# Kernel tuning notes

Hardware: AMD Instinct MI355X
Metric: run time of the kernel (lower is better)

The kernel has to match this reference:

```python
import jax, jax.numpy as jnp
import numpy as np

H = 16       # num heads
D = 80       # head dim
HID = H * D  # 1280
S = 4096     # total tokens


def setup_inputs() -> dict:
    key = jax.random.key(0)
    ks = jax.random.split(key, 6)
    x = jax.random.normal(ks[0], (S, HID), dtype=jnp.float32)
    # 4 images of 1024 patch tokens each
    cu_seqlens = jnp.array([0, 1024, 2048, 3072, 4096], dtype=jnp.int32)
    rotary_pos_emb = jax.random.normal(ks[1], (S, D // 2), dtype=jnp.float32)
    sc = 1.0 / np.sqrt(HID)
    qkv_w = jax.random.normal(ks[2], (3 * HID, HID), dtype=jnp.float32) * sc
    qkv_b = jax.random.normal(ks[3], (3 * HID,), dtype=jnp.float32) * 0.02
    proj_w = jax.random.normal(ks[4], (HID, HID), dtype=jnp.float32) * sc
    proj_b = jax.random.normal(ks[5], (HID,), dtype=jnp.float32) * 0.02
    return {"x": x, "cu_seqlens": cu_seqlens, "rotary_pos_emb": rotary_pos_emb,
            "qkv_w": qkv_w, "qkv_b": qkv_b, "proj_w": proj_w, "proj_b": proj_b}


def _rotate_half(t):
    t1, t2 = jnp.split(t, 2, axis=-1)
    return jnp.concatenate([-t2, t1], axis=-1)


def _apply_rope(t, freqs):
    # t: [S, H, D], freqs: [S, D//2] -> cos/sin broadcast as [S, 1, D]
    emb = jnp.concatenate([freqs, freqs], axis=-1)[:, None, :]
    return t * jnp.cos(emb) + _rotate_half(t) * jnp.sin(emb)


def reference(x, cu_seqlens, rotary_pos_emb, qkv_w, qkv_b, proj_w, proj_b):
    seq_len = x.shape[0]
    qkv = (x @ qkv_w.T + qkv_b).reshape(seq_len, 3, H, D)
    q, k, v = qkv[:, 0], qkv[:, 1], qkv[:, 2]  # each [S, H, D]
    q = _apply_rope(q, rotary_pos_emb)
    k = _apply_rope(k, rotary_pos_emb)
    # block-diagonal mask from cu_seqlens: same segment -> 0, else dtype min
    seg = jnp.searchsorted(cu_seqlens[1:], jnp.arange(seq_len), side='right')
    neg = jnp.finfo(q.dtype).min
    attn_mask = jnp.where(seg[:, None] == seg[None, :], 0.0, neg).astype(q.dtype)
    scores = jnp.einsum('shd,thd->hst', q, k) / jnp.sqrt(jnp.asarray(D, q.dtype))
    scores = scores + attn_mask[None]
    attn = jax.nn.softmax(scores.astype(jnp.float32), axis=-1).astype(q.dtype)
    out = jnp.einsum('hst,thd->shd', attn, v).reshape(seq_len, H * D)
    return out @ proj_w.T + proj_b
```

## Files before the change

kernel.cpp:

```cpp
#include <hip/hip_runtime.h>

typedef _Float16 f16;
typedef __attribute__((ext_vector_type(8))) _Float16 f16x8;
typedef __attribute__((ext_vector_type(4))) float f32x4;

#define SEQ   4096
#define NH    16
#define HD    80
#define HIDN  1280
#define DP    96

#define KSZ   3328
#define VSZ   4480
#define HSZ   (2*KSZ + 2*VSZ)

#define KQ   1280
#define NQ   3840
#define NIT  10

__device__ __forceinline__ void gload16(const void* g, void* l) {
  __builtin_amdgcn_global_load_lds(
      (const __attribute__((address_space(1))) unsigned int*)g,
      (__attribute__((address_space(3))) unsigned int*)l, 16, 0, 0);
}

__device__ __forceinline__ unsigned pk2(float a, float b) {
  return __builtin_bit_cast(unsigned, __builtin_amdgcn_cvt_pkrtz(a, b));
}
__device__ __forceinline__ f16x8 bc16(uint4 u) { return __builtin_bit_cast(f16x8, u); }

#define BAR() __builtin_amdgcn_s_barrier()
#define VMCNT(n) do { asm volatile("s_waitcnt vmcnt(" #n ")" ::: "memory"); \
                      __builtin_amdgcn_sched_barrier(0); } while (0)
#define STG(Lb, g, buf, h, kt)                                                  \
  do {                                                                          \
    gload16((g) + (size_t)((h) * 128) * KQ + (kt) * 64,                         \
            (Lb) + (buf) * 16384 + ((h) * 128) * 64 + w * 512);                 \
    gload16((g) + (size_t)((h) * 128 + 64) * KQ + (kt) * 64,                    \
            (Lb) + (buf) * 16384 + ((h) * 128 + 64) * 64 + w * 512);            \
  } while (0)
#define MFQ(IOFF, JOFF, BB)                                                     \
  do {                                                                          \
    __builtin_amdgcn_s_setprio(1);                                              \
    _Pragma("unroll")                                                           \
    for (int i_ = 0; i_ < 4; i_++)                                              \
      _Pragma("unroll")                                                         \
      for (int j_ = 0; j_ < 2; j_++)                                            \
        _Pragma("unroll")                                                       \
        for (int s_ = 0; s_ < 2; s_++)                                          \
          acc[i_ + IOFF][j_ + JOFF] = __builtin_amdgcn_mfma_f32_16x16x32_f16(   \
              a[i_][s_], BB[j_][s_], acc[i_ + IOFF][j_ + JOFF], 0, 0, 0);       \
    __builtin_amdgcn_s_setprio(0);                                              \
  } while (0)

__global__ __launch_bounds__(256) void cvt3_kernel(const float* __restrict__ s0,
                                                   const float* __restrict__ s1,
                                                   const float* __restrict__ s2,
                                                   f16* __restrict__ d0,
                                                   f16* __restrict__ d1,
                                                   f16* __restrict__ d2,
                                                   int n0, int n1, int n2) {
  long i = (long)(blockIdx.x * 256 + threadIdx.x) * 8;
  const float* s; f16* d;
  if (i < n0)                { s = s0 + i;            d = d0 + i; }
  else if (i < n0 + n1)      { s = s1 + (i - n0);     d = d1 + (i - n0); }
  else if (i < n0 + n1 + n2) { s = s2 + (i - n0 - n1); d = d2 + (i - n0 - n1); }
  else return;
  f32x4 v0 = *(const f32x4*)(s);
  f32x4 v1 = *(const f32x4*)(s + 4);
  f16x8 o;
#pragma unroll
  for (int j = 0; j < 4; j++) { o[j] = (f16)v0[j]; o[4 + j] = (f16)v1[j]; }
  *(f16x8*)(d) = o;
}

__global__ __launch_bounds__(512, 2) void qkv_gemm8(const f16* __restrict__ A,
                                                    const f16* __restrict__ B,
                                                    const float* __restrict__ bias,
                                                    f16* __restrict__ C) {
  __shared__ __align__(16) f16 LA[2 * 16384];
  __shared__ __align__(16) f16 LB[2 * 16384];
  const int tid = threadIdx.x, w = tid >> 6, l = tid & 63;
  const int bid = (blockIdx.x & 7) * 30 + (blockIdx.x >> 3);
  const int bx = bid % 15, by = bid / 15;
  const int m0 = by * 256, n0 = bx * 256;
  const int wm = (w >> 2) * 128, wn = (w & 3) * 64;
  const int fr = l & 15, fq = l >> 4;
  const int rx = fr & 7;
  const int cA0 = (fq ^ rx) * 8;
  const int cA1 = ((4 + fq) ^ rx) * 8;

  const int srow = w * 8 + (l >> 3);
  const int scol = ((l & 7) ^ (l >> 3)) * 8;
  const f16* gA = A + (size_t)(m0 + srow) * KQ + scol;
  const f16* gB = B + (size_t)(n0 + srow) * KQ + scol;

  f32x4 acc[8][4] = {};
  f16x8 a[4][2], b0[2][2], b1[2][2];

  STG(LA, gA, 0, 0, 0); STG(LA, gA, 0, 1, 0);
  STG(LB, gB, 0, 0, 0); STG(LB, gB, 0, 1, 0);
  STG(LB, gB, 1, 0, 1); STG(LB, gB, 1, 1, 1);
  VMCNT(4);
  BAR();

  for (int it = 0; it < NIT; ++it) {
    const int t = 2 * it;
    const bool lastit = (it == NIT - 1);

#pragma unroll
    for (int i = 0; i < 4; i++) {
      a[i][0] = *(const f16x8*)(LA + (wm + i * 16 + fr) * 64 + cA0);
      a[i][1] = *(const f16x8*)(LA + (wm + i * 16 + fr) * 64 + cA1);
    }
#pragma unroll
    for (int j = 0; j < 2; j++) {
      b0[j][0] = *(const f16x8*)(LB + (wn + j * 16 + fr) * 64 + cA0);
      b0[j][1] = *(const f16x8*)(LB + (wn + j * 16 + fr) * 64 + cA1);
    }
    STG(LA, gA, 1, 0, t + 1);
    BAR(); MFQ(0, 0, b0); BAR();

#pragma unroll
    for (int j = 0; j < 2; j++) {
      b1[j][0] = *(const f16x8*)(LB + (wn + 32 + j * 16 + fr) * 64 + cA0);
      b1[j][1] = *(const f16x8*)(LB + (wn + 32 + j * 16 + fr) * 64 + cA1);
    }
    STG(LA, gA, 1, 1, t + 1);
    BAR(); MFQ(0, 2, b1); BAR();

#pragma unroll
    for (int i = 0; i < 4; i++) {
      a[i][0] = *(const f16x8*)(LA + (wm + 64 + i * 16 + fr) * 64 + cA0);
      a[i][1] = *(const f16x8*)(LA + (wm + 64 + i * 16 + fr) * 64 + cA1);
    }
    if (!lastit) { STG(LB, gB, 0, 0, t + 2); }
    BAR(); MFQ(4, 0, b0); BAR();

    if (!lastit) { STG(LB, gB, 0, 1, t + 2); VMCNT(4); }
    else         { VMCNT(0); }
    BAR(); MFQ(4, 2, b1); BAR();

#pragma unroll
    for (int i = 0; i < 4; i++) {
      a[i][0] = *(const f16x8*)(LA + 16384 + (wm + i * 16 + fr) * 64 + cA0);
      a[i][1] = *(const f16x8*)(LA + 16384 + (wm + i * 16 + fr) * 64 + cA1);
    }
#pragma unroll
    for (int j = 0; j < 2; j++) {
      b0[j][0] = *(const f16x8*)(LB + 16384 + (wn + j * 16 + fr) * 64 + cA0);
      b0[j][1] = *(const f16x8*)(LB + 16384 + (wn + j * 16 + fr) * 64 + cA1);
    }
    if (!lastit) { STG(LA, gA, 0, 0, t + 2); }
    BAR(); MFQ(0, 0, b0); BAR();

#pragma unroll
    for (int j = 0; j < 2; j++) {
      b1[j][0] = *(const f16x8*)(LB + 16384 + (wn + 32 + j * 16 + fr) * 64 + cA0);
      b1[j][1] = *(const f16x8*)(LB + 16384 + (wn + 32 + j * 16 + fr) * 64 + cA1);
    }
    if (!lastit) { STG(LA, gA, 0, 1, t + 2); }
    BAR(); MFQ(0, 2, b1); BAR();

#pragma unroll
    for (int i = 0; i < 4; i++) {
      a[i][0] = *(const f16x8*)(LA + 16384 + (wm + 64 + i * 16 + fr) * 64 + cA0);
      a[i][1] = *(const f16x8*)(LA + 16384 + (wm + 64 + i * 16 + fr) * 64 + cA1);
    }
    if (!lastit) { STG(LB, gB, 1, 0, t + 3); }
    BAR(); MFQ(4, 0, b0); BAR();

    if (!lastit) { STG(LB, gB, 1, 1, t + 3); VMCNT(4); }
    BAR(); MFQ(4, 2, b1); BAR();
  }

#pragma unroll
  for (int i = 0; i < 8; i++) {
    const int row = m0 + wm + i * 16 + fq * 4;
#pragma unroll
    for (int j = 0; j < 4; j++) {
      const int col = n0 + wn + j * 16 + fr;
      const float bv = bias[col];
#pragma unroll
      for (int q = 0; q < 4; q++)
        C[(size_t)(row + q) * NQ + col] = (f16)(acc[i][j][q] + bv);
    }
  }
}

template<int OUT_F32>
__global__ __launch_bounds__(256) void gemm_bt64(const f16* __restrict__ A,
                                                 const f16* __restrict__ B,
                                                 const float* __restrict__ bias,
                                                 void* __restrict__ C,
                                                 int M, int N, int K) {
  __shared__ __align__(16) f16 AsF[8192];
  __shared__ __align__(16) f16 BsF[8192];
  const int tid = threadIdx.x;
  const int w = tid >> 6, l = tid & 63;
  const int m0 = blockIdx.y * 128, n0 = blockIdx.x * 128;
  const int wm = (w >> 1) * 64, wn = (w & 1) * 64;
  const int fr = l & 15, fg = (l >> 4) * 8;

  size_t aoff[4], boff[4];
#pragma unroll
  for (int i = 0; i < 4; i++) {
    const int d = i * 256 + tid;
    const int sub = d >> 9, dd = d & 511;
    const int r = dd >> 2, c = (dd & 3) + sub * 4;
    aoff[i] = (size_t)(m0 + r) * K + c * 8;
    boff[i] = (size_t)(n0 + r) * K + c * 8;
  }

  f32x4 acc[4][4] = {};

  for (int k0 = 0; k0 < K; k0 += 64) {
    if (k0) __syncthreads();
#pragma unroll
    for (int i = 0; i < 4; i++) gload16(A + aoff[i] + k0, AsF + (i * 256 + tid) * 8);
#pragma unroll
    for (int i = 0; i < 4; i++) gload16(B + boff[i] + k0, BsF + (i * 256 + tid) * 8);
    __syncthreads();
    f16x8 af[4][2], bf[4][2];
#pragma unroll
    for (int i = 0; i < 4; i++)
#pragma unroll
      for (int s = 0; s < 2; s++) {
        af[i][s] = *(const f16x8*)(AsF + s * 4096 + (wm + i * 16 + fr) * 32 + fg);
        bf[i][s] = *(const f16x8*)(BsF + s * 4096 + (wn + i * 16 + fr) * 32 + fg);
      }
#pragma unroll
    for (int i = 0; i < 4; i++)
#pragma unroll
      for (int j = 0; j < 4; j++)
#pragma unroll
        for (int s = 0; s < 2; s++)
          acc[i][j] = __builtin_amdgcn_mfma_f32_16x16x32_f16(af[i][s], bf[j][s], acc[i][j], 0, 0, 0);
  }

  const int q4 = (l >> 4) * 4;
#pragma unroll
  for (int i = 0; i < 4; i++) {
    const int row = m0 + wm + i * 16 + q4;
#pragma unroll
    for (int j = 0; j < 4; j++) {
      const int col = n0 + wn + j * 16 + fr;
      const float bv = bias[col];
#pragma unroll
      for (int q = 0; q < 4; q++) {
        float v = acc[i][j][q] + bv;
        if (OUT_F32) ((float*)C)[(size_t)(row + q) * N + col] = v;
        else         ((f16*)C)[(size_t)(row + q) * N + col] = (f16)v;
      }
    }
  }
}

#define RPB 1280
__global__ __launch_bounds__(256) void prep_kernel(const f16* __restrict__ qkvb,
                                                   const float* __restrict__ rpe,
                                                   f16* __restrict__ qh,
                                                   f16* __restrict__ kh,
                                                   f16* __restrict__ vt) {
  __shared__ f16 tile[HD][65];
  const int b = blockIdx.x;
  if (b < RPB) {
    const float SCLT = 0.1118033988749895f * 1.4426950408889634f;
    const int t = b * 256 + threadIdx.x;
    const int d8 = (t % 5) * 8;
    const int h = (t / 5) % NH;
    const int s = t / (5 * NH);
    const f32x4 f0 = *(const f32x4*)(rpe + s * 40 + d8);
    const f32x4 f1 = *(const f32x4*)(rpe + s * 40 + d8 + 4);
    const f16* base = qkvb + (size_t)s * (3 * HIDN) + h * HD;
    const f16x8 q0 = *(const f16x8*)(base + d8);
    const f16x8 q1 = *(const f16x8*)(base + 40 + d8);
    const f16x8 k0 = *(const f16x8*)(base + HIDN + d8);
    const f16x8 k1 = *(const f16x8*)(base + HIDN + 40 + d8);
    f16x8 oq0, oq1, ok0, ok1;
#pragma unroll
    for (int j = 0; j < 8; j++) {
      const float fv = (j < 4) ? f0[j] : f1[j - 4];
      float sn, cs;
      __sincosf(fv, &sn, &cs);
      const float a = (float)q0[j], bq = (float)q1[j];
      oq0[j] = (f16)((a * cs - bq * sn) * SCLT);
      oq1[j] = (f16)((bq * cs + a * sn) * SCLT);
      const float ka = (float)k0[j], kb = (float)k1[j];
      ok0[j] = (f16)(ka * cs - kb * sn);
      ok1[j] = (f16)(kb * cs + ka * sn);
    }
    const size_t ob = ((size_t)h * SEQ + s) * DP;
    *(f16x8*)(qh + ob + d8)      = oq0;
    *(f16x8*)(qh + ob + 40 + d8) = oq1;
    *(f16x8*)(kh + ob + d8)      = ok0;
    *(f16x8*)(kh + ob + 40 + d8) = ok1;
    if (d8 == 32) {
      const f16x8 z = {};
      *(f16x8*)(qh + ob + 80) = z; *(f16x8*)(qh + ob + 88) = z;
      *(f16x8*)(kh + ob + 80) = z; *(f16x8*)(kh + ob + 88) = z;
    }
  } else {
    const int bb = b - RPB;
    const int h = bb >> 6;
    const int s0 = (bb & 63) * 64;
    for (int idx = threadIdx.x; idx < 64 * HD; idx += 256) {
      const int sr = idx / HD, d = idx % HD;
      tile[d][sr] = qkvb[(size_t)(s0 + sr) * (3 * HIDN) + 2 * HIDN + h * HD + d];
    }
    __syncthreads();
    for (int idx = threadIdx.x; idx < HD * 64; idx += 256) {
      const int d = idx >> 6, sc = idx & 63;
      const int blk = sc >> 5, s = sc & 31, g = s >> 3, j = s & 7;
      const int act = blk * 32 + ((j < 4) ? (4 * g + j) : (16 + 4 * g + (j - 4)));
      vt[((size_t)h * HD + d) * SEQ + s0 + sc] = tile[d][act];
    }
  }
}

__global__ __launch_bounds__(512, 2) void attn_kernel(const f16* __restrict__ qh,
                                                      const f16* __restrict__ kh,
                                                      const f16* __restrict__ vt,
                                                      const int* __restrict__ cu,
                                                      f16* __restrict__ ao) {
  __shared__ __align__(16) f16 smem[2 * HSZ];
  const int tid = threadIdx.x, w = tid >> 6, l = tid & 63;
  const int grp = w >> 2, wq = w & 3;
  const int bid = blockIdx.x;
  const int g = bid & 63, ib = bid >> 6;
  const int h = g >> 2;
  const int qblk = ((g & 3) * 4 + ib) * 256;
  int seg = 0;
  while (cu[seg + 1] <= qblk) seg++;
  const int kvb = cu[seg], kve = cu[seg + 1];
  const int nt = (kve - kvb + 63) >> 6;
  const int fr = l & 15, fg = (l >> 4) * 8;
  const int row0 = qblk + wq * 64;

  const f16* qb = qh + ((size_t)h * SEQ + row0 + fr) * DP + fg;
  f16x8 aq[4][3];
#pragma unroll
  for (int u = 0; u < 4; u++)
#pragma unroll
    for (int kk = 0; kk < 3; kk++)
      aq[u][kk] = *(const f16x8*)(qb + u * 16 * DP + kk * 32);

  const int k0g = tid / 384, k0r = (tid % 384) / 12, k0c = tid % 12;
  const int k1r = (128 + tid) / 12, k1c = (128 + tid) % 12;
  const int v0g = tid / 320, v0r = (tid % 320) / 4, v0c = tid & 3;
  const int v1r = (192 + tid) >> 2, v1c = (192 + tid) & 3;
  const f16* kp0 = kh + ((size_t)h * SEQ + kvb + k0g * 32 + k0r) * DP + k0c * 8;
  const f16* kp1 = kh + ((size_t)h * SEQ + kvb + 32 + k1r) * DP + k1c * 8;
  const f16* vp0 = vt + ((size_t)h * HD + v0r) * SEQ + kvb + v0g * 32 + v0c * 8;
  const f16* vp1 = vt + ((size_t)h * HD + v1r) * SEQ + kvb + 32 + v1c * 8;
  const int dK0 = k0g * KSZ + k0r * 104 + k0c * 8;
  const int dK1 = KSZ + k1r * 104 + k1c * 8;
  const int dV0 = 2 * KSZ + v0g * VSZ + v0r * 56 + v0c * 8;
  const int dV1 = 2 * KSZ + VSZ + v1r * 56 + v1c * 8;

  float m = -1e30f;
  float ls[4] = {0.f, 0.f, 0.f, 0.f};
  f32x4 o[4][5] = {};

  uint4 rk0, rk1, rv0, rv1;
  rk0 = *(const uint4*)kp0;
  if (tid < 256) rk1 = *(const uint4*)kp1;
  rv0 = *(const uint4*)vp0;
  if (tid < 128) rv1 = *(const uint4*)vp1;
  *(uint4*)(smem + dK0) = rk0;
  if (tid < 256) *(uint4*)(smem + dK1) = rk1;
  *(uint4*)(smem + dV0) = rv0;
  if (tid < 128) *(uint4*)(smem + dV1) = rv1;
  __syncthreads();

  for (int t = 0; t < nt; t++) {
    const int p = t & 1;
    const int off = (t + 1) * 64;
    const bool more = (t + 1 < nt);

    if (more) {
      rk0 = *(const uint4*)(kp0 + (size_t)off * DP);
      if (tid < 256) rk1 = *(const uint4*)(kp1 + (size_t)off * DP);
      rv0 = *(const uint4*)(vp0 + off);
      if (tid < 128) rv1 = *(const uint4*)(vp1 + off);
    }

    const f16* myK = smem + p * HSZ + grp * KSZ;
    const f16* myV = smem + p * HSZ + 2 * KSZ + grp * VSZ;

    f32x4 s[4][2] = {};
    __builtin_amdgcn_s_setprio(1);
#pragma unroll
    for (int kk = 0; kk < 3; kk++) {
      const f16x8 k0 = *(const f16x8*)(myK + fr * 104 + kk * 32 + fg);
      const f16x8 k1 = *(const f16x8*)(myK + (16 + fr) * 104 + kk * 32 + fg);
#pragma unroll
      for (int u = 0; u < 4; u++) {
        s[u][0] = __builtin_amdgcn_mfma_f32_16x16x32_f16(k0, aq[u][kk], s[u][0], 0, 0, 0);
        s[u][1] = __builtin_amdgcn_mfma_f32_16x16x32_f16(k1, aq[u][kk], s[u][1], 0, 0, 0);
      }
    }
    __builtin_amdgcn_s_setprio(0);

    float pmax = s[0][0][0];
#pragma unroll
    for (int u = 0; u < 4; u++)
#pragma unroll
      for (int j = 0; j < 4; j++)
        pmax = fmaxf(pmax, fmaxf(s[u][0][j], s[u][1][j]));
    if (__any(pmax > m + 8.f)) {
      float tmax = pmax;
      tmax = fmaxf(tmax, __shfl_xor(tmax, 1));
      tmax = fmaxf(tmax, __shfl_xor(tmax, 2));
      tmax = fmaxf(tmax, __shfl_xor(tmax, 4));
      tmax = fmaxf(tmax, __shfl_xor(tmax, 8));
      tmax = fmaxf(tmax, __shfl_xor(tmax, 16));
      tmax = fmaxf(tmax, __shfl_xor(tmax, 32));
      const float aa = __builtin_amdgcn_exp2f(m - tmax);
      m = tmax;
#pragma unroll
      for (int u = 0; u < 4; u++) {
        ls[u] *= aa;
#pragma unroll
        for (int dt = 0; dt < 5; dt++)
#pragma unroll
          for (int j = 0; j < 4; j++) o[u][dt][j] *= aa;
      }
    }

    f16x8 pa[4];
#pragma unroll
    for (int u = 0; u < 4; u++) {
#pragma unroll
      for (int r = 0; r < 4; r++) {
        s[u][0][r] = __builtin_amdgcn_exp2f(s[u][0][r] - m);
        s[u][1][r] = __builtin_amdgcn_exp2f(s[u][1][r] - m);
        ls[u] += s[u][0][r] + s[u][1][r];
      }
      uint4 ua;
      ua.x = pk2(s[u][0][0], s[u][0][1]); ua.y = pk2(s[u][0][2], s[u][0][3]);
      ua.z = pk2(s[u][1][0], s[u][1][1]); ua.w = pk2(s[u][1][2], s[u][1][3]);
      pa[u] = bc16(ua);
    }

    __builtin_amdgcn_s_setprio(1);
#pragma unroll
    for (int dt = 0; dt < 5; dt++) {
      const f16x8 bv = *(const f16x8*)(myV + (dt * 16 + fr) * 56 + fg);
#pragma unroll
      for (int u = 0; u < 4; u++)
        o[u][dt] = __builtin_amdgcn_mfma_f32_16x16x32_f16(pa[u], bv, o[u][dt], 0, 0, 0);
    }
    __builtin_amdgcn_s_setprio(0);

    if (more) {
      f16* dst = smem + (1 - p) * HSZ;
      *(uint4*)(dst + dK0) = rk0;
      if (tid < 256) *(uint4*)(dst + dK1) = rk1;
      *(uint4*)(dst + dV0) = rv0;
      if (tid < 128) *(uint4*)(dst + dV1) = rv1;
    }
    __syncthreads();
  }

#pragma unroll
  for (int u = 0; u < 4; u++) {
    ls[u] += __shfl_xor(ls[u], 16);
    ls[u] += __shfl_xor(ls[u], 32);
  }

  float* mb = (float*)smem;
  float aA = 1.f, aB = 0.f;
  if (grp == 1) {
    float* dst = mb + (wq * 64 + l) * 43;
    dst[0] = m; dst[1] = ls[0]; dst[2] = ls[1];
#pragma unroll
    for (int u = 0; u < 2; u++)
#pragma unroll
      for (int dt = 0; dt < 5; dt++)
#pragma unroll
        for (int j = 0; j < 4; j++)
          dst[3 + u * 20 + dt * 4 + j] = o[u][dt][j];
  }
  __syncthreads();
  if (grp == 0) {
    const float* src = mb + (wq * 64 + l) * 43;
    const float mB = src[0];
    const float M = fmaxf(m, mB);
    aA = __builtin_amdgcn_exp2f(m - M);
    aB = __builtin_amdgcn_exp2f(mB - M);
    ls[0] = ls[0] * aA + src[1] * aB;
    ls[1] = ls[1] * aA + src[2] * aB;
#pragma unroll
    for (int u = 0; u < 2; u++)
#pragma unroll
      for (int dt = 0; dt < 5; dt++)
#pragma unroll
        for (int j = 0; j < 4; j++)
          o[u][dt][j] = o[u][dt][j] * aA + src[3 + u * 20 + dt * 4 + j] * aB;
  }
  __syncthreads();
  if (grp == 1) {
    float* dst = mb + (wq * 64 + l) * 42;
    dst[0] = ls[2]; dst[1] = ls[3];
#pragma unroll
    for (int u = 2; u < 4; u++)
#pragma unroll
      for (int dt = 0; dt < 5; dt++)
#pragma unroll
        for (int j = 0; j < 4; j++)
          dst[2 + (u - 2) * 20 + dt * 4 + j] = o[u][dt][j];
  }
  __syncthreads();
  if (grp == 0) {
    const float* src = mb + (wq * 64 + l) * 42;
    ls[2] = ls[2] * aA + src[0] * aB;
    ls[3] = ls[3] * aA + src[1] * aB;
#pragma unroll
    for (int u = 2; u < 4; u++)
#pragma unroll
      for (int dt = 0; dt < 5; dt++)
#pragma unroll
        for (int j = 0; j < 4; j++)
          o[u][dt][j] = o[u][dt][j] * aA + src[2 + (u - 2) * 20 + dt * 4 + j] * aB;

#pragma unroll
    for (int u = 0; u < 4; u++) {
      const float inv = 1.0f / ls[u];
      float iv[4];
#pragma unroll
      for (int j = 0; j < 4; j++) {
        const int srcl = (l & 48) | ((l >> 4) * 4 + j);
        iv[j] = __shfl(inv, srcl);
      }
      const int orow = row0 + u * 16 + (l >> 4) * 4;
#pragma unroll
      for (int dt = 0; dt < 5; dt++)
#pragma unroll
        for (int j = 0; j < 4; j++)
          ao[(size_t)(orow + j) * HIDN + h * HD + dt * 16 + fr] = (f16)(o[u][dt][j] * iv[j]);
    }
  }
}

extern "C" void kernel_launch(void* const* d_in, const int* in_sizes, int n_in,
                              void* d_out, int out_size, void* d_ws, size_t ws_size,
                              hipStream_t stream) {
  const float* x      = (const float*)d_in[0];
  const int*   cu     = (const int*)d_in[1];
  const float* rpe    = (const float*)d_in[2];
  const float* qkv_w  = (const float*)d_in[3];
  const float* qkv_b  = (const float*)d_in[4];
  const float* proj_w = (const float*)d_in[5];
  const float* proj_b = (const float*)d_in[6];

  char* ws = (char*)d_ws;
  f16* xb    = (f16*)(ws);
  f16* wqkv  = (f16*)(ws + 10485760);
  f16* wproj = (f16*)(ws + 20316160);
  f16* qkvb  = (f16*)(ws + 23592960);
  f16* qh    = (f16*)(ws + 55050240);
  f16* kh    = (f16*)(ws + 67633152);
  f16* vt    = (f16*)(ws + 80216064);
  f16* ao    = xb;

  const int n0 = SEQ * HIDN, n1 = 3 * HIDN * HIDN, n2 = HIDN * HIDN;
  cvt3_kernel<<<(n0 + n1 + n2) / (256 * 8), 256, 0, stream>>>(
      x, qkv_w, proj_w, xb, wqkv, wproj, n0, n1, n2);

  qkv_gemm8<<<240, 512, 0, stream>>>(xb, wqkv, qkv_b, qkvb);

  prep_kernel<<<RPB + 1024, 256, 0, stream>>>(qkvb, rpe, qh, kh, vt);

  attn_kernel<<<256, 512, 0, stream>>>(qh, kh, vt, cu, ao);

  gemm_bt64<1><<<dim3(HIDN / 128, SEQ / 128), 256, 0, stream>>>(
      ao, wproj, proj_b, d_out, SEQ, HIDN, HIDN);
}
```

Before: 132.8 us.

## Halve QKV GEMM k-tile to raise occupancy and remap proj GEMM blocks by XCD

The QKV GEMM now stages 32-wide k-slices instead of 64-wide, halving LDS use and A/B fragment registers. The launch bound goes from 2 to 4 blocks per CU, with a new XOR swizzle and twice as many loop iterations. The output projection GEMM switches to a 1D grid with an XCD-aware block remap, so neighbouring tiles land on the same chiplet for L2 reuse. The cost is more barriers and global-load issues per unit of compute in the QKV loop, and a shorter prefetch distance in k.

Result: slower. 479.6 us (+261.1%).

```diff
diff --git a/kernel.cpp b/kernel.cpp
--- a/kernel.cpp
+++ b/kernel.cpp
@@ -16,7 +16,7 @@
 
 #define KQ   1280
 #define NQ   3840
-#define NIT  10
+#define NIT  20
 
 __device__ __forceinline__ void gload16(const void* g, void* l) {
   __builtin_amdgcn_global_load_lds(
@@ -32,24 +32,18 @@
 #define BAR() __builtin_amdgcn_s_barrier()
 #define VMCNT(n) do { asm volatile("s_waitcnt vmcnt(" #n ")" ::: "memory"); \
                       __builtin_amdgcn_sched_barrier(0); } while (0)
-#define STG(Lb, g, buf, h, kt)                                                  \
-  do {                                                                          \
-    gload16((g) + (size_t)((h) * 128) * KQ + (kt) * 64,                         \
-            (Lb) + (buf) * 16384 + ((h) * 128) * 64 + w * 512);                 \
-    gload16((g) + (size_t)((h) * 128 + 64) * KQ + (kt) * 64,                    \
-            (Lb) + (buf) * 16384 + ((h) * 128 + 64) * 64 + w * 512);            \
-  } while (0)
-#define MFQ(IOFF, JOFF, BB)                                                     \
+#define STG32(Lb, g, buf, h, kt)                                                \
+  gload16((g) + (size_t)((h) * 128) * KQ + (kt) * 32,                           \
+          (Lb) + (buf) * 8192 + (h) * 4096 + w * 512)
+#define MFQ32(IOFF, JOFF, BB)                                                   \
   do {                                                                          \
     __builtin_amdgcn_s_setprio(1);                                              \
     _Pragma("unroll")                                                           \
     for (int i_ = 0; i_ < 4; i_++)                                              \
       _Pragma("unroll")                                                         \
       for (int j_ = 0; j_ < 2; j_++)                                            \
-        _Pragma("unroll")                                                       \
-        for (int s_ = 0; s_ < 2; s_++)                                          \
-          acc[i_ + IOFF][j_ + JOFF] = __builtin_amdgcn_mfma_f32_16x16x32_f16(   \
-              a[i_][s_], BB[j_][s_], acc[i_ + IOFF][j_ + JOFF], 0, 0, 0);       \
+        acc[i_ + IOFF][j_ + JOFF] = __builtin_amdgcn_mfma_f32_16x16x32_f16(     \
+            a[i_], BB[j_], acc[i_ + IOFF][j_ + JOFF], 0, 0, 0);                 \
     __builtin_amdgcn_s_setprio(0);                                              \
   } while (0)
 
@@ -74,34 +68,32 @@
   *(f16x8*)(d) = o;
 }
 
-__global__ __launch_bounds__(512, 2) void qkv_gemm8(const f16* __restrict__ A,
+__global__ __launch_bounds__(512, 4) void qkv_gemm8(const f16* __restrict__ A,
                                                     const f16* __restrict__ B,
                                                     const float* __restrict__ bias,
                                                     f16* __restrict__ C) {
-  __shared__ __align__(16) f16 LA[2 * 16384];
-  __shared__ __align__(16) f16 LB[2 * 16384];
+  __shared__ __align__(16) f16 LA[2 * 8192];
+  __shared__ __align__(16) f16 LB[2 * 8192];
   const int tid = threadIdx.x, w = tid >> 6, l = tid & 63;
   const int bid = (blockIdx.x & 7) * 30 + (blockIdx.x >> 3);
   const int bx = bid % 15, by = bid / 15;
   const int m0 = by * 256, n0 = bx * 256;
   const int wm = (w >> 2) * 128, wn = (w & 3) * 64;
   const int fr = l & 15, fq = l >> 4;
-  const int rx = fr & 7;
-  const int cA0 = (fq ^ rx) * 8;
-  const int cA1 = ((4 + fq) ^ rx) * 8;
-
-  const int srow = w * 8 + (l >> 3);
-  const int scol = ((l & 7) ^ (l >> 3)) * 8;
+  const int cA = (fq ^ ((fr >> 1) & 3)) * 8;
+
+  const int srow = tid >> 2;
+  const int scol = ((tid & 3) ^ ((tid >> 3) & 3)) * 8;
   const f16* gA = A + (size_t)(m0 + srow) * KQ + scol;
   const f16* gB = B + (size_t)(n0 + srow) * KQ + scol;
 
   f32x4 acc[8][4] = {};
-  f16x8 a[4][2], b0[2][2], b1[2][2];
-
-  STG(LA, gA, 0, 0, 0); STG(LA, gA, 0, 1, 0);
-  STG(LB, gB, 0, 0, 0); STG(LB, gB, 0, 1, 0);
-  STG(LB, gB, 1, 0, 1); STG(LB, gB, 1, 1, 1);
-  VMCNT(4);
+  f16x8 a[4], b0[2], b1[2];
+
+  STG32(LA, gA, 0, 0, 0); STG32(LA, gA, 0, 1, 0);
+  STG32(LB, gB, 0, 0, 0); STG32(LB, gB, 0, 1, 0);
+  STG32(LB, gB, 1, 0, 1); STG32(LB, gB, 1, 1, 1);
+  VMCNT(2);
   BAR();
 
   for (int it = 0; it < NIT; ++it) {
@@ -109,69 +101,53 @@
     const bool lastit = (it == NIT - 1);
 
 #pragma unroll
-    for (int i = 0; i < 4; i++) {
-      a[i][0] = *(const f16x8*)(LA + (wm + i * 16 + fr) * 64 + cA0);
-      a[i][1] = *(const f16x8*)(LA + (wm + i * 16 + fr) * 64 + cA1);
-    }
-#pragma unroll
-    for (int j = 0; j < 2; j++) {
-      b0[j][0] = *(const f16x8*)(LB + (wn + j * 16 + fr) * 64 + cA0);
-      b0[j][1] = *(const f16x8*)(LB + (wn + j * 16 + fr) * 64 + cA1);
-    }
-    STG(LA, gA, 1, 0, t + 1);
-    BAR(); MFQ(0, 0, b0); BAR();
-
-#pragma unroll
-    for (int j = 0; j < 2; j++) {
-      b1[j][0] = *(const f16x8*)(LB + (wn + 32 + j * 16 + fr) * 64 + cA0);
-      b1[j][1] = *(const f16x8*)(LB + (wn + 32 + j * 16 + fr) * 64 + cA1);
-    }
-    STG(LA, gA, 1, 1, t + 1);
-    BAR(); MFQ(0, 2, b1); BAR();
-
-#pragma unroll
-    for (int i = 0; i < 4; i++) {
-      a[i][0] = *(const f16x8*)(LA + (wm + 64 + i * 16 + fr) * 64 + cA0);
-      a[i][1] = *(const f16x8*)(LA + (wm + 64 + i * 16 + fr) * 64 + cA1);
-    }
-    if (!lastit) { STG(LB, gB, 0, 0, t + 2); }
-    BAR(); MFQ(4, 0, b0); BAR();
-
-    if (!lastit) { STG(LB, gB, 0, 1, t + 2); VMCNT(4); }
+    for (int i = 0; i < 4; i++)
+      a[i] = *(const f16x8*)(LA + (wm + i * 16 + fr) * 32 + cA);
+#pragma unroll
+    for (int j = 0; j < 2; j++)
+      b0[j] = *(const f16x8*)(LB + (wn + j * 16 + fr) * 32 + cA);
+    STG32(LA, gA, 1, 0, t + 1);
+    BAR(); MFQ32(0, 0, b0); BAR();
+
+#pragma unroll
+    for (int j = 0; j < 2; j++)
+      b1[j] = *(const f16x8*)(LB + (wn + 32 + j * 16 + fr) * 32 + cA);
+    STG32(LA, gA, 1, 1, t + 1);
+    BAR(); MFQ32(0, 2, b1); BAR();
+
+#pragma unroll
+    for (int i = 0; i < 4; i++)
+      a[i] = *(const f16x8*)(LA + (wm + 64 + i * 16 + fr) * 32 + cA);
+    if (!lastit) { STG32(LB, gB, 0, 0, t + 2); }
+    BAR(); MFQ32(4, 0, b0); BAR();
+
+    if (!lastit) { STG32(LB, gB, 0, 1, t + 2); VMCNT(2); }
     else         { VMCNT(0); }
-    BAR(); MFQ(4, 2, b1); BAR();
-
-#pragma unroll
-    for (int i = 0; i < 4; i++) {
-      a[i][0] = *(const f16x8*)(LA + 16384 + (wm + i * 16 + fr) * 64 + cA0);
-      a[i][1] = *(const f16x8*)(LA + 16384 + (wm + i * 16 + fr) * 64 + cA1);
-    }
-#pragma unroll
-    for (int j = 0; j < 2; j++) {
-      b0[j][0] = *(const f16x8*)(LB + 16384 + (wn + j * 16 + fr) * 64 + cA0);
-      b0[j][1] = *(const f16x8*)(LB + 16384 + (wn + j * 16 + fr) * 64 + cA1);
-    }
-    if (!lastit) { STG(LA, gA, 0, 0, t + 2); }
-    BAR(); MFQ(0, 0, b0); BAR();
-
-#pragma unroll
-    for (int j = 0; j < 2; j++) {
-      b1[j][0] = *(const f16x8*)(LB + 16384 + (wn + 32 + j * 16 + fr) * 64 + cA0);
-      b1[j][1] = *(const f16x8*)(LB + 16384 + (wn + 32 + j * 16 + fr) * 64 + cA1);
-    }
-    if (!lastit) { STG(LA, gA, 0, 1, t + 2); }
-    BAR(); MFQ(0, 2, b1); BAR();
-
-#pragma unroll
-    for (int i = 0; i < 4; i++) {
-      a[i][0] = *(const f16x8*)(LA + 16384 + (wm + 64 + i * 16 + fr) * 64 + cA0);
-      a[i][1] = *(const f16x8*)(LA + 16384 + (wm + 64 + i * 16 + fr) * 64 + cA1);
-    }
-    if (!lastit) { STG(LB, gB, 1, 0, t + 3); }
-    BAR(); MFQ(4, 0, b0); BAR();
-
-    if (!lastit) { STG(LB, gB, 1, 1, t + 3); VMCNT(4); }
-    BAR(); MFQ(4, 2, b1); BAR();
+    BAR(); MFQ32(4, 2, b1); BAR();
+
+#pragma unroll
+    for (int i = 0; i < 4; i++)
+      a[i] = *(const f16x8*)(LA + 8192 + (wm + i * 16 + fr) * 32 + cA);
+#pragma unroll
+    for (int j = 0; j < 2; j++)
+      b0[j] = *(const f16x8*)(LB + 8192 + (wn + j * 16 + fr) * 32 + cA);
+    if (!lastit) { STG32(LA, gA, 0, 0, t + 2); }
+    BAR(); MFQ32(0, 0, b0); BAR();
+
+#pragma unroll
+    for (int j = 0; j < 2; j++)
+      b1[j] = *(const f16x8*)(LB + 8192 + (wn + 32 + j * 16 + fr) * 32 + cA);
+    if (!lastit) { STG32(LA, gA, 0, 1, t + 2); }
+    BAR(); MFQ32(0, 2, b1); BAR();
+
+#pragma unroll
+    for (int i = 0; i < 4; i++)
+      a[i] = *(const f16x8*)(LA + 8192 + (wm + 64 + i * 16 + fr) * 32 + cA);
+    if (!lastit) { STG32(LB, gB, 1, 0, t + 3); }
+    BAR(); MFQ32(4, 0, b0); BAR();
+
+    if (!lastit) { STG32(LB, gB, 1, 1, t + 3); VMCNT(2); }
+    BAR(); MFQ32(4, 2, b1); BAR();
   }
 
 #pragma unroll
@@ -193,12 +169,14 @@
                                                  const f16* __restrict__ B,
                                                  const float* __restrict__ bias,
                                                  void* __restrict__ C,
-                                                 int M, int N, int K) {
+                                                 int M, int N, int K,
+                                                 int nbx, int cpx) {
   __shared__ __align__(16) f16 AsF[8192];
   __shared__ __align__(16) f16 BsF[8192];
   const int tid = threadIdx.x;
   const int w = tid >> 6, l = tid & 63;
-  const int m0 = blockIdx.y * 128, n0 = blockIdx.x * 128;
+  const int bid = (blockIdx.x & 7) * cpx + (blockIdx.x >> 3);
+  const int m0 = (bid / nbx) * 128, n0 = (bid % nbx) * 128;
   const int wm = (w >> 1) * 64, wn = (w & 1) * 64;
   const int fr = l & 15, fg = (l >> 4) * 8;
 
@@ -574,6 +552,6 @@
 
   attn_kernel<<<256, 512, 0, stream>>>(qh, kh, vt, cu, ao);
 
-  gemm_bt64<1><<<dim3(HIDN / 128, SEQ / 128), 256, 0, stream>>>(
-      ao, wproj, proj_b, d_out, SEQ, HIDN, HIDN);
-}
+  gemm_bt64<1><<<320, 256, 0, stream>>>(
+      ao, wproj, proj_b, d_out, SEQ, HIDN, HIDN, 10, 40);
+}
```
